# Kernel optimization log

Hardware: AMD Instinct MI355X
Metric: run time of the kernel (lower is better)

## Reference

```python
import jax, jax.numpy as jnp
import numpy as np


def setup_inputs() -> dict:
    key = jax.random.key(0)
    k1, k2, k3, k4, k5 = jax.random.split(key, 5)
    B, Te, Td, De, Dd = 8, 256, 256, 512, 512
    return {
        "encoder_out_seq": jax.random.normal(k1, (B, Te, De), dtype=jnp.float32),
        "decoder_out_seq": jax.random.normal(k2, (B, Td, Dd), dtype=jnp.float32),
        "W_a": jax.random.normal(k3, (De, De), dtype=jnp.float32) * 0.05,
        "U_a": jax.random.normal(k4, (Dd, De), dtype=jnp.float32) * 0.05,
        "V_a": jax.random.normal(k5, (De, 1), dtype=jnp.float32) * 0.05,
    }


def reference(encoder_out_seq, decoder_out_seq, W_a, U_a, V_a):
    # Bahdanau additive attention, fully vectorized over decoder timesteps
    # (replaces the two sequential K.rnn scans in the original).
    Ws = jnp.einsum('bte,ef->btf', encoder_out_seq, W_a)   # [B,Te,De]
    Uh = jnp.einsum('bqd,df->bqf', decoder_out_seq, U_a)   # [B,Td,De]
    # scores[b,q,t] = tanh(Ws[b,t,:] + Uh[b,q,:]) . V_a
    scores = jnp.einsum('bqtf,f->bqt',
                        jnp.tanh(Ws[:, None, :, :] + Uh[:, :, None, :]),
                        V_a[:, 0])                          # [B,Td,Te]
    e = jax.nn.softmax(scores, axis=-1)                     # attention weights
    c = jnp.einsum('bqt,btf->bqf', e, encoder_out_seq)      # context vectors
    return (c, e)
```

## Files before the change

### kernel.cpp

```cpp
#include <hip/hip_runtime.h>

#define NB 8
#define TE 256
#define TD 256
#define DE 512
#define QT 4

#define K2SCALE 2.8853900817779268f

typedef short bf16x8 __attribute__((ext_vector_type(8)));
typedef float f32x4 __attribute__((ext_vector_type(4)));
typedef float f32x2 __attribute__((ext_vector_type(2)));
typedef unsigned short u16x8 __attribute__((ext_vector_type(8)));

static __device__ __forceinline__ unsigned short f2bf(float x) {
  unsigned int u = __float_as_uint(x);
  u += 0x7fffu + ((u >> 16) & 1u);
  return (unsigned short)(u >> 16);
}

static __device__ __forceinline__ void split8(
    const float4& x0, const float4& x1, u16x8& h, u16x8& l) {
  float xs[8] = {x0.x, x0.y, x0.z, x0.w, x1.x, x1.y, x1.z, x1.w};
  #pragma unroll
  for (int j = 0; j < 8; ++j) {
    unsigned short hh = f2bf(xs[j]);
    float hf = __uint_as_float((unsigned int)hh << 16);
    h[j] = hh;
    l[j] = f2bf(xs[j] - hf);
  }
}

template <int CTRL>
static __device__ __forceinline__ float dpp_mov(float x) {
  return __int_as_float(__builtin_amdgcn_update_dpp(
      0, __float_as_int(x), CTRL, 0xf, 0xf, true));
}

__global__ __launch_bounds__(256) void convB(
    const float* __restrict__ w0, unsigned short* __restrict__ h0, unsigned short* __restrict__ l0,
    const float* __restrict__ w1, unsigned short* __restrict__ h1, unsigned short* __restrict__ l1)
{
  const float* W = blockIdx.z ? w1 : w0;
  unsigned short* H = blockIdx.z ? h1 : h0;
  unsigned short* L = blockIdx.z ? l1 : l0;
  __shared__ unsigned short sh[32][33], sl[32][33];
  const int t = threadIdx.x;
  const int k0 = blockIdx.y * 32, n0 = blockIdx.x * 32;
  const int r = t >> 3, c = (t & 7) * 4;
  float4 x = *(const float4*)(W + (size_t)(k0 + r) * DE + n0 + c);
  float xs[4] = {x.x, x.y, x.z, x.w};
  #pragma unroll
  for (int j = 0; j < 4; ++j) {
    unsigned short hh = f2bf(xs[j]);
    float hf = __uint_as_float((unsigned int)hh << 16);
    sh[r][c + j] = hh;
    sl[r][c + j] = f2bf(xs[j] - hf);
  }
  __syncthreads();
  ushort4 oh, ol;
  oh.x = sh[c + 0][r]; oh.y = sh[c + 1][r]; oh.z = sh[c + 2][r]; oh.w = sh[c + 3][r];
  ol.x = sl[c + 0][r]; ol.y = sl[c + 1][r]; ol.z = sl[c + 2][r]; ol.w = sl[c + 3][r];
  *(ushort4*)(H + (size_t)(n0 + r) * DE + k0 + c) = oh;
  *(ushort4*)(L + (size_t)(n0 + r) * DE + k0 + c) = ol;
}

__global__ __launch_bounds__(256) void gemm_mfma(
    const float* __restrict__ A0,
    const unsigned short* __restrict__ BH0, const unsigned short* __restrict__ BL0,
    float* __restrict__ C0,
    const float* __restrict__ A1,
    const unsigned short* __restrict__ BH1, const unsigned short* __restrict__ BL1,
    float* __restrict__ C1)
{
  const float*          A  = blockIdx.z ? A1  : A0;
  const unsigned short* BH = blockIdx.z ? BH1 : BH0;
  const unsigned short* BL = blockIdx.z ? BL1 : BL0;
  float*                C  = blockIdx.z ? C1  : C0;
  const int tid  = threadIdx.x;
  const int lane = tid & 63;
  const int wave = tid >> 6;
  const int wm = wave >> 1, wn = wave & 1;
  const int g = lane >> 4, r16 = lane & 15;
  const int m0 = blockIdx.y * 64, n0 = blockIdx.x * 64;
  __shared__ __align__(16) unsigned short Ah[2][64][40], Al[2][64][40];
  __shared__ __align__(16) unsigned short Bh[2][64][40], Bl[2][64][40];
  const int arow = tid >> 2;
  const int apart = (tid & 3) * 8;

  float4 a00, a01;
  u16x8 pb, plb;
#define LOADTILE(KT) do {                                                   \
    const size_t ko = (size_t)(KT) * 32 + apart;                            \
    const float* pa_ = A + (size_t)(m0 + arow) * 512 + ko;                  \
    a00 = *(const float4*)pa_;  a01 = *(const float4*)(pa_ + 4);            \
    pb  = *(const u16x8*)(BH + (size_t)(n0 + arow) * 512 + ko);             \
    plb = *(const u16x8*)(BL + (size_t)(n0 + arow) * 512 + ko);             \
  } while (0)
#define STORETILE(BUF) do {                                                 \
    u16x8 h0_, l0_;                                                         \
    split8(a00, a01, h0_, l0_);                                             \
    *(u16x8*)&Ah[BUF][arow][apart] = h0_;                                   \
    *(u16x8*)&Al[BUF][arow][apart] = l0_;                                   \
    *(u16x8*)&Bh[BUF][arow][apart] = pb;                                    \
    *(u16x8*)&Bl[BUF][arow][apart] = plb;                                   \
  } while (0)

  f32x4 accm[2][2], acce[2][2];
  #pragma unroll
  for (int mt = 0; mt < 2; ++mt)
    #pragma unroll
    for (int nt = 0; nt < 2; ++nt) {
      accm[mt][nt] = (f32x4){0.f, 0.f, 0.f, 0.f};
      acce[mt][nt] = (f32x4){0.f, 0.f, 0.f, 0.f};
    }

  LOADTILE(0);
  STORETILE(0);
  __syncthreads();

  for (int kt = 0; kt < 16; ++kt) {
    const int cur = kt & 1;
    if (kt + 1 < 16) LOADTILE(kt + 1);
    bf16x8 ah[2], al[2], bh[2], bl[2];
    #pragma unroll
    for (int mt = 0; mt < 2; ++mt) {
      ah[mt] = *(const bf16x8*)&Ah[cur][wm * 32 + mt * 16 + r16][g * 8];
      al[mt] = *(const bf16x8*)&Al[cur][wm * 32 + mt * 16 + r16][g * 8];
    }
    #pragma unroll
    for (int nt = 0; nt < 2; ++nt) {
      bh[nt] = *(const bf16x8*)&Bh[cur][wn * 32 + nt * 16 + r16][g * 8];
      bl[nt] = *(const bf16x8*)&Bl[cur][wn * 32 + nt * 16 + r16][g * 8];
    }
    #pragma unroll
    for (int mt = 0; mt < 2; ++mt)
      #pragma unroll
      for (int nt = 0; nt < 2; ++nt) {
        accm[mt][nt] = __builtin_amdgcn_mfma_f32_16x16x32_bf16(ah[mt], bh[nt], accm[mt][nt], 0, 0, 0);
        acce[mt][nt] = __builtin_amdgcn_mfma_f32_16x16x32_bf16(al[mt], bh[nt], acce[mt][nt], 0, 0, 0);
        acce[mt][nt] = __builtin_amdgcn_mfma_f32_16x16x32_bf16(ah[mt], bl[nt], acce[mt][nt], 0, 0, 0);
      }
    if (kt + 1 < 16) STORETILE(cur ^ 1);
    __syncthreads();
  }
#undef LOADTILE
#undef STORETILE

  #pragma unroll
  for (int mt = 0; mt < 2; ++mt)
    #pragma unroll
    for (int nt = 0; nt < 2; ++nt)
      #pragma unroll
      for (int jj = 0; jj < 4; ++jj) {
        float vsum = accm[mt][nt][jj] + acce[mt][nt][jj];
        int row = m0 + wm * 32 + mt * 16 + g * 4 + jj;
        int col = n0 + wn * 32 + nt * 16 + r16;
        C[(size_t)row * 512 + col] = __builtin_amdgcn_exp2f(vsum * K2SCALE);
      }
}

__global__ __launch_bounds__(512, 4) void attn(
    const float* __restrict__ ws, const float* __restrict__ uh,
    const float* __restrict__ enc, const float* __restrict__ va,
    float* __restrict__ out_c, float* __restrict__ out_e)
{
  const int tid  = threadIdx.x;
  const int wave = tid >> 6;
  const int lane = tid & 63;
  const int b  = blockIdx.x & 7;
  const int q0 = (blockIdx.x >> 3) * QT;
  __shared__ float s_sc[QT][TE];
  __shared__ float red[3][QT][DE];
  const int fbase = lane * 8;

  float4 v0 = *(const float4*)(va + fbase);
  float4 v1 = *(const float4*)(va + fbase + 4);
  float v[8] = {v0.x, v0.y, v0.z, v0.w, v1.x, v1.y, v1.z, v1.w};
  f32x2 vP[8];
  #pragma unroll
  for (int j = 0; j < 8; ++j) vP[j] = (f32x2){v[j], v[j]};

  f32x2 euP[2][8];
  #pragma unroll
  for (int p = 0; p < 2; ++p) {
    const float* up0 = uh + (size_t)(b * TD + q0 + 2 * p) * DE + fbase;
    const float* up1 = up0 + DE;
    float4 a0 = *(const float4*)(up0);
    float4 a1 = *(const float4*)(up0 + 4);
    float4 b0 = *(const float4*)(up1);
    float4 b1 = *(const float4*)(up1 + 4);
    float ea[8] = {a0.x, a0.y, a0.z, a0.w, a1.x, a1.y, a1.z, a1.w};
    float eb[8] = {b0.x, b0.y, b0.z, b0.w, b1.x, b1.y, b1.z, b1.w};
    #pragma unroll
    for (int j = 0; j < 8; ++j) euP[p][j] = (f32x2){ea[j], eb[j]};
  }
  const f32x2 one2 = {1.f, 1.f};

  const int t0 = wave * 32;
  const float* wp = ws + (size_t)(b * TE + t0) * DE + fbase;
  float4 w0 = *(const float4*)(wp);
  float4 w1 = *(const float4*)(wp + 4);
  for (int t = t0; t < t0 + 32; ++t) {
    float cw[8] = {w0.x, w0.y, w0.z, w0.w, w1.x, w1.y, w1.z, w1.w};
    wp += DE;
    w0 = *(const float4*)(wp);
    w1 = *(const float4*)(wp + 4);
    f32x2 cw2[8];
    #pragma unroll
    for (int j = 0; j < 8; ++j) cw2[j] = (f32x2){cw[j], cw[j]};
    float a[QT];
    #pragma unroll
    for (int p = 0; p < 2; ++p) {
      f32x2 A0 = __builtin_elementwise_fma(cw2[0], euP[p][0], one2);
      f32x2 A1 = __builtin_elementwise_fma(cw2[1], euP[p][1], one2);
      f32x2 A2 = __builtin_elementwise_fma(cw2[2], euP[p][2], one2);
      f32x2 A3 = __builtin_elementwise_fma(cw2[3], euP[p][3], one2);
      f32x2 B0 = __builtin_elementwise_fma(cw2[4], euP[p][4], one2);
      f32x2 B1 = __builtin_elementwise_fma(cw2[5], euP[p][5], one2);
      f32x2 B2 = __builtin_elementwise_fma(cw2[6], euP[p][6], one2);
      f32x2 B3 = __builtin_elementwise_fma(cw2[7], euP[p][7], one2);
      f32x2 n1 = __builtin_elementwise_fma(vP[1], A0, vP[0] * A1);
      f32x2 d1 = A0 * A1;
      f32x2 n2 = __builtin_elementwise_fma(vP[3], A2, vP[2] * A3);
      f32x2 d2 = A2 * A3;
      f32x2 N1 = __builtin_elementwise_fma(n2, d1, n1 * d2);
      f32x2 D1 = d1 * d2;
      f32x2 n3 = __builtin_elementwise_fma(vP[5], B0, vP[4] * B1);
      f32x2 d3 = B0 * B1;
      f32x2 n4 = __builtin_elementwise_fma(vP[7], B2, vP[6] * B3);
      f32x2 d4 = B2 * B3;
      f32x2 N2 = __builtin_elementwise_fma(n4, d3, n3 * d4);
      f32x2 D2 = d3 * d4;
      float s0 = N1.x * __builtin_amdgcn_rcpf(D1.x);
      a[2 * p + 0] = fmaf(N2.x, __builtin_amdgcn_rcpf(D2.x), s0);
      float s1 = N1.y * __builtin_amdgcn_rcpf(D1.y);
      a[2 * p + 1] = fmaf(N2.y, __builtin_amdgcn_rcpf(D2.y), s1);
    }
    {
      const bool h1 = lane & 1;
      float m0 = h1 ? a[1] : a[0], o0 = h1 ? a[0] : a[1];
      float m1 = h1 ? a[3] : a[2], o1 = h1 ? a[2] : a[3];
      float r0 = m0 + dpp_mov<0xB1>(o0);
      float r1 = m1 + dpp_mov<0xB1>(o1);
      const bool h2 = lane & 2;
      float mm = h2 ? r1 : r0, oo = h2 ? r0 : r1;
      float r = mm + dpp_mov<0x4E>(oo);
      r += dpp_mov<0x124>(r);
      r += dpp_mov<0x128>(r);
      r += __shfl_xor(r, 16, 64);
      r += __shfl_xor(r, 32, 64);
      if (lane < QT) s_sc[lane][t] = -2.f * r;
    }
  }
  __syncthreads();

  if (wave < QT) {
    const int r = wave;
    float x[4];
    #pragma unroll
    for (int i = 0; i < 4; ++i) x[i] = s_sc[r][lane + 64 * i];
    float m = fmaxf(fmaxf(x[0], x[1]), fmaxf(x[2], x[3]));
    #pragma unroll
    for (int off = 32; off >= 1; off >>= 1) m = fmaxf(m, __shfl_xor(m, off, 64));
    const float L2E = 1.4426950408889634f;
    float ssum = 0.f;
    #pragma unroll
    for (int i = 0; i < 4; ++i) { x[i] = __builtin_amdgcn_exp2f((x[i] - m) * L2E); ssum += x[i]; }
    #pragma unroll
    for (int off = 32; off >= 1; off >>= 1) ssum += __shfl_xor(ssum, off, 64);
    float inv = 1.f / ssum;
    float* oe = out_e + (size_t)(b * TD + q0 + r) * TE;
    #pragma unroll
    for (int i = 0; i < 4; ++i) {
      float e = x[i] * inv;
      s_sc[r][lane + 64 * i] = e;
      oe[lane + 64 * i] = e;
    }
  }
  __syncthreads();

  {
    const int fgrp = tid >> 7;
    const int f4   = (tid & 127) * 4;
    float4 c[QT];
    #pragma unroll
    for (int q = 0; q < QT; ++q) c[q] = make_float4(0.f, 0.f, 0.f, 0.f);
    const float* eb = enc + (size_t)b * TE * DE + f4;
    const int tb = fgrp * 64;
    #pragma unroll 4
    for (int t = tb; t < tb + 64; ++t) {
      float4 ee = *(const float4*)(eb + (size_t)t * DE);
      #pragma unroll
      for (int q = 0; q < QT; ++q) {
        float w = s_sc[q][t];
        c[q].x = fmaf(w, ee.x, c[q].x);
        c[q].y = fmaf(w, ee.y, c[q].y);
        c[q].z = fmaf(w, ee.z, c[q].z);
        c[q].w = fmaf(w, ee.w, c[q].w);
      }
    }
    if (fgrp > 0) {
      #pragma unroll
      for (int q = 0; q < QT; ++q) *(float4*)&red[fgrp - 1][q][f4] = c[q];
    }
    __syncthreads();
    if (fgrp == 0) {
      #pragma unroll
      for (int q = 0; q < QT; ++q) {
        float4 r1 = *(const float4*)&red[0][q][f4];
        float4 r2 = *(const float4*)&red[1][q][f4];
        float4 r3 = *(const float4*)&red[2][q][f4];
        c[q].x += (r1.x + r2.x) + r3.x;
        c[q].y += (r1.y + r2.y) + r3.y;
        c[q].z += (r1.z + r2.z) + r3.z;
        c[q].w += (r1.w + r2.w) + r3.w;
        *(float4*)(out_c + (size_t)(b * TD + q0 + q) * DE + f4) = c[q];
      }
    }
  }
}

extern "C" void kernel_launch(void* const* d_in, const int* in_sizes, int n_in,
                              void* d_out, int out_size, void* d_ws, size_t ws_size,
                              hipStream_t stream) {
  const float* enc = (const float*)d_in[0];
  const float* dec = (const float*)d_in[1];
  const float* Wa  = (const float*)d_in[2];
  const float* Ua  = (const float*)d_in[3];
  const float* Va  = (const float*)d_in[4];
  float* out_c = (float*)d_out;
  float* out_e = out_c + (size_t)NB * TD * DE;

  float* ws = (float*)d_ws;
  float* uh = ws + 1048576;
  unsigned short* BHw = (unsigned short*)(uh + 1048576);
  unsigned short* BLw = BHw + 262144;
  unsigned short* BHu = BLw + 262144;
  unsigned short* BLu = BHu + 262144;

  convB<<<dim3(16, 16, 2), dim3(256), 0, stream>>>(Wa, BHw, BLw, Ua, BHu, BLu);
  gemm_mfma<<<dim3(8, 32, 2), dim3(256), 0, stream>>>(
      enc, BHw, BLw, ws, dec, BHu, BLu, uh);
  attn<<<dim3(NB * (TD / QT)), dim3(512), 0, stream>>>(
      ws, uh, enc, Va, out_c, out_e);
}
```

Measured before the change: 65.61 us.

## Split score computation into separate kernel with finer-grained grid

Moves the tanh-score computation out of the fused attention kernel into its own kernel. The new kernel uses 256-thread blocks, each handling 64 encoder timesteps, so the grid is four times larger. Scores are written to a global workspace, and a second kernel then does the softmax and context reduction. This aims for higher occupancy and better load balance on the dominant score phase. The cost is an extra kernel launch and a global round trip for the score matrix.

New measurement: 106.6 us. 1.62x slower.

```diff
diff --git a/kernel.cpp b/kernel.cpp
--- a/kernel.cpp
+++ b/kernel.cpp
@@ -160,18 +160,19 @@
       }
 }
 
-__global__ __launch_bounds__(512, 4) void attn(
+__global__ __launch_bounds__(256, 8) void scores(
     const float* __restrict__ ws, const float* __restrict__ uh,
-    const float* __restrict__ enc, const float* __restrict__ va,
-    float* __restrict__ out_c, float* __restrict__ out_e)
+    const float* __restrict__ va, float* __restrict__ out_s)
 {
   const int tid  = threadIdx.x;
   const int wave = tid >> 6;
   const int lane = tid & 63;
-  const int b  = blockIdx.x & 7;
-  const int q0 = (blockIdx.x >> 3) * QT;
-  __shared__ float s_sc[QT][TE];
-  __shared__ float red[3][QT][DE];
+  const int blk  = blockIdx.x;
+  const int b    = blk & 7;
+  const int rest = blk >> 3;
+  const int q0   = (rest & 63) * QT;
+  const int tq   = rest >> 6;
+  const int t0   = tq * 64 + wave * 16;
   const int fbase = lane * 8;
 
   float4 v0 = *(const float4*)(va + fbase);
@@ -197,11 +198,10 @@
   }
   const f32x2 one2 = {1.f, 1.f};
 
-  const int t0 = wave * 32;
   const float* wp = ws + (size_t)(b * TE + t0) * DE + fbase;
   float4 w0 = *(const float4*)(wp);
   float4 w1 = *(const float4*)(wp + 4);
-  for (int t = t0; t < t0 + 32; ++t) {
+  for (int t = t0; t < t0 + 16; ++t) {
     float cw[8] = {w0.x, w0.y, w0.z, w0.w, w1.x, w1.y, w1.z, w1.w};
     wp += DE;
     w0 = *(const float4*)(wp);
@@ -250,16 +250,30 @@
       r += dpp_mov<0x128>(r);
       r += __shfl_xor(r, 16, 64);
       r += __shfl_xor(r, 32, 64);
-      if (lane < QT) s_sc[lane][t] = -2.f * r;
-    }
-  }
-  __syncthreads();
+      if (lane < QT)
+        out_s[(size_t)(b * TD + q0 + lane) * TE + t] = -2.f * r;
+    }
+  }
+}
+
+__global__ __launch_bounds__(512) void attn2(
+    const float* __restrict__ gs, const float* __restrict__ enc,
+    float* __restrict__ out_c, float* __restrict__ out_e)
+{
+  const int tid  = threadIdx.x;
+  const int wave = tid >> 6;
+  const int lane = tid & 63;
+  const int b  = blockIdx.x & 7;
+  const int q0 = (blockIdx.x >> 3) * QT;
+  __shared__ float s_sc[QT][TE];
+  __shared__ float red[3][QT][DE];
 
   if (wave < QT) {
     const int r = wave;
+    const float* row = gs + (size_t)(b * TD + q0 + r) * TE;
     float x[4];
     #pragma unroll
-    for (int i = 0; i < 4; ++i) x[i] = s_sc[r][lane + 64 * i];
+    for (int i = 0; i < 4; ++i) x[i] = row[lane + 64 * i];
     float m = fmaxf(fmaxf(x[0], x[1]), fmaxf(x[2], x[3]));
     #pragma unroll
     for (int off = 32; off >= 1; off >>= 1) m = fmaxf(m, __shfl_xor(m, off, 64));
@@ -338,10 +352,11 @@
   unsigned short* BLw = BHw + 262144;
   unsigned short* BHu = BLw + 262144;
   unsigned short* BLu = BHu + 262144;
+  float* gsc = (float*)(BLu + 262144);
 
   convB<<<dim3(16, 16, 2), dim3(256), 0, stream>>>(Wa, BHw, BLw, Ua, BHu, BLu);
   gemm_mfma<<<dim3(8, 32, 2), dim3(256), 0, stream>>>(
       enc, BHw, BLw, ws, dec, BHu, BLu, uh);
-  attn<<<dim3(NB * (TD / QT)), dim3(512), 0, stream>>>(
-      ws, uh, enc, Va, out_c, out_e);
-}
+  scores<<<dim3(NB * (TD / QT) * 4), dim3(256), 0, stream>>>(ws, uh, Va, gsc);
+  attn2<<<dim3(NB * (TD / QT)), dim3(512), 0, stream>>>(gsc, enc, out_c, out_e);
+}
```
